# Optimization experiments

Hardware: AMD Instinct MI355X
Metric: run time of the kernel (lower is better)

## Reference

```python
import jax, jax.numpy as jnp
import numpy as np

B, L, T = 4, 512, 4096
HID, NH = 1024, 16
HD = HID // NH
MAX_POS = 4096
BASE = 10000.0


def _cos_sin(dim, max_pos, base):
    inv_freq = 1.0 / base ** (jnp.arange(0, dim, 2, dtype=jnp.float32) / dim)
    t = jnp.arange(max_pos, dtype=jnp.float32)
    freqs = jnp.einsum('i,j->ij', t, inv_freq)
    emb = jnp.concatenate([freqs, freqs], axis=-1)  # [max_pos, dim]
    return jnp.cos(emb), jnp.sin(emb)


def _rotate_half(x):
    x1, x2 = x[..., : x.shape[-1] // 2], x[..., x.shape[-1] // 2:]
    return jnp.concatenate([-x2, x1], axis=-1)


def setup_inputs() -> dict:
    key = jax.random.key(0)
    ks = jax.random.split(key, 12)
    s = 0.02
    inp = {
        'latents': jax.random.normal(ks[0], (B, L, HID), jnp.float32),
        'target': jax.random.normal(ks[1], (B, T, HID), jnp.float32),
        'target_mask': jax.random.randint(ks[2], (B, T), 0, 2).astype(bool),
        'target_timestamp': jnp.sort(jax.random.randint(ks[3], (B, T), 0, MAX_POS), axis=-1),
        'Wq': jax.random.normal(ks[4], (HID, HID), jnp.float32) * s,
        'bq': jnp.zeros((HID,), jnp.float32),
        'Wk': jax.random.normal(ks[5], (HID, HID), jnp.float32) * s,
        'bk': jnp.zeros((HID,), jnp.float32),
        'Wv': jax.random.normal(ks[6], (HID, HID), jnp.float32) * s,
        'bv': jnp.zeros((HID,), jnp.float32),
        'Wo': jax.random.normal(ks[7], (HID, HID), jnp.float32) * s,
        'bo': jnp.zeros((HID,), jnp.float32),
    }
    return inp


def reference(latents, target, target_mask, target_timestamp, Wq, bq, Wk, bk, Wv, bv, Wo, bo):
    cos, sin = _cos_sin(HD, MAX_POS, BASE)  # [MAX_POS, HD]
    # latents_timestamp: arange(L) * (max-1)/(L-1), cast to int
    lat_ts = (jnp.arange(L, dtype=jnp.float32) * (MAX_POS - 1) / (L - 1)).astype(jnp.int64)
    lat_ts = jnp.broadcast_to(lat_ts[None, :], (B, L))

    # QKV projections (torch Linear: x @ W.T + b)
    q = (latents @ Wq.T + bq).reshape(B, L, NH, HD).transpose(0, 2, 1, 3)  # [B,H,L,D]
    k = (target @ Wk.T + bk).reshape(B, T, NH, HD).transpose(0, 2, 1, 3)   # [B,H,T,D]
    v = (target @ Wv.T + bv).reshape(B, T, NH, HD).transpose(0, 2, 1, 3)

    # RoPE with gathered timestamps; unsqueeze over head dim
    cq, sq = cos[lat_ts][:, None], sin[lat_ts][:, None]          # [B,1,L,D]
    ck, sk = cos[target_timestamp][:, None], sin[target_timestamp][:, None]  # [B,1,T,D]
    q = q * cq + _rotate_half(q) * sq
    k = k * ck + _rotate_half(k) * sk

    # SDPA with boolean attn mask (True = attend)
    scores = jnp.einsum('bhld,bhtd->bhlt', q, k) / jnp.sqrt(jnp.float32(HD))
    bias = jnp.where(target_mask[:, None, None, :], 0.0, -jnp.inf).astype(scores.dtype)
    attn = jax.nn.softmax(scores + bias, axis=-1)
    out = jnp.einsum('bhlt,bhtd->bhld', attn, v)  # [B,H,L,D]
    out = out.transpose(0, 2, 1, 3).reshape(B, L, HID)
    return out @ Wo.T + bo
```

## Files before the change

kernel.cpp:

```cpp
#include <hip/hip_runtime.h>

#define B_ 4
#define L_ 512
#define T_ 4096
#define NH_ 16
#define HD_ 64

using f32x4 = __attribute__((ext_vector_type(4))) float;
using bf16x8 = __attribute__((ext_vector_type(8))) short;
using u32x4 = __attribute__((ext_vector_type(4))) unsigned int;

__device__ __forceinline__ unsigned short f2bf(float x) {
  unsigned int u = __builtin_bit_cast(unsigned int, x);
  u += 0x7fffu + ((u >> 16) & 1u);
  return (unsigned short)(u >> 16);
}

__device__ __forceinline__ unsigned cvtpk(float lo, float hi) {
  unsigned r;
  asm("v_cvt_pk_bf16_f32 %0, %1, %2" : "=v"(r) : "v"(lo), "v"(hi));
  return r;
}

__device__ __forceinline__ u32x4 cvt8(const float4& a, const float4& b) {
  u32x4 r;
  r[0] = (unsigned)f2bf(a.x) | ((unsigned)f2bf(a.y) << 16);
  r[1] = (unsigned)f2bf(a.z) | ((unsigned)f2bf(a.w) << 16);
  r[2] = (unsigned)f2bf(b.x) | ((unsigned)f2bf(b.y) << 16);
  r[3] = (unsigned)f2bf(b.z) | ((unsigned)f2bf(b.w) << 16);
  return r;
}

__device__ __forceinline__ void gload16(const void* g, void* l) {
  __builtin_amdgcn_global_load_lds(
      (const __attribute__((address_space(1))) unsigned int*)g,
      (__attribute__((address_space(3))) unsigned int*)l, 16, 0, 0);
}

#define BC8(x) __builtin_bit_cast(bf16x8, (x))

struct CvtArgs {
  const float* src[6];
  unsigned short* dst[6];
  int cum[7];
};

__global__ void cvt_bf16(CvtArgs a, int total, float* __restrict__ cost,
                         float* __restrict__ sint) {
  if (blockIdx.x >= 2048) {
    const int idx = (blockIdx.x - 2048) * 256 + threadIdx.x;
    const int pos = idx >> 5, i = idx & 31;
    const float inv = 1.0f / powf(10000.0f, (float)(2 * i) * (1.0f / 64.0f));
    const float f = (float)pos * inv;
    cost[idx] = cosf(f);
    sint[idx] = sinf(f);
    return;
  }
  for (int g = blockIdx.x * 256 + threadIdx.x; g < total; g += 2048 * 256) {
    int r = 0;
#pragma unroll
    for (int q = 0; q < 5; ++q) r += (g >= a.cum[q + 1]);
    const int lc = g - a.cum[r];
    const float4* s = (const float4*)a.src[r] + (size_t)lc * 2;
    float4 x0 = s[0], x1 = s[1];
    *((u32x4*)a.dst[r] + lc) = cvt8(x0, x1);
  }
}

template <int EPI>
__global__ __launch_bounds__(256, 2) void gemm_bf(
    const unsigned short* __restrict__ A, const unsigned short* __restrict__ Wb,
    const float* __restrict__ bias, void* __restrict__ outp,
    const float* __restrict__ cost, const float* __restrict__ sint,
    const int* __restrict__ ts) {
  __shared__ u32x4 lsA[2][512];
  __shared__ u32x4 lsB[2][512];
  const int tid = threadIdx.x;
  const int mt = blockIdx.x >> 3, nt = blockIdx.x & 7;
  const int mBase = mt << 7, nBase = nt << 7;
  const int lane = tid & 63, wid = tid >> 6;
  const int wr = wid >> 1, wc = wid & 1;
  const int lr = lane & 15, lg = lane >> 4;

  f32x4 acc[4][4];
#pragma unroll
  for (int m = 0; m < 4; ++m)
#pragma unroll
    for (int n = 0; n < 4; ++n) acc[m][n] = (f32x4){0.f, 0.f, 0.f, 0.f};

  auto stage = [&](int bi, int kt) {
    const int ko = kt * 32;
#pragma unroll
    for (int j2 = 0; j2 < 2; ++j2) {
      const int j = wid * 2 + j2;
      const int row = (j & 1) * 64 + lane;
      const int kg = j >> 1;
      gload16(A + (size_t)(mBase + row) * 1024 + ko + kg * 8,
              (unsigned short*)lsA[bi] + j * 512);
      gload16(Wb + (size_t)(nBase + row) * 1024 + ko + kg * 8,
              (unsigned short*)lsB[bi] + j * 512);
    }
  };

  stage(0, 0);
  __syncthreads();
  int cur = 0;
  for (int kt = 0; kt < 32; ++kt) {
    if (kt < 31) stage(cur ^ 1, kt + 1);
    const u32x4* As = lsA[cur];
    const u32x4* Bs = lsB[cur];
    bf16x8 af[4], bfr[4];
#pragma unroll
    for (int m = 0; m < 4; ++m) af[m] = BC8(As[lg * 128 + wr * 64 + m * 16 + lr]);
#pragma unroll
    for (int n = 0; n < 4; ++n) bfr[n] = BC8(Bs[lg * 128 + wc * 64 + n * 16 + lr]);
#pragma unroll
    for (int m = 0; m < 4; ++m)
#pragma unroll
      for (int n = 0; n < 4; ++n)
        acc[m][n] = __builtin_amdgcn_mfma_f32_16x16x32_bf16(af[m], bfr[n], acc[m][n], 0, 0, 0);
    __syncthreads();
    cur ^= 1;
  }

  float bv[4];
#pragma unroll
  for (int n = 0; n < 4; ++n) bv[n] = bias[nBase + wc * 64 + n * 16 + lr];

  if (EPI == 3) {
    float* Of = (float*)outp;
#pragma unroll
    for (int m = 0; m < 4; ++m)
#pragma unroll
      for (int r = 0; r < 4; ++r) {
        const int gR = mBase + wr * 64 + m * 16 + lg * 4 + r;
#pragma unroll
        for (int n = 0; n < 4; ++n)
          Of[(size_t)gR * 1024 + nBase + wc * 64 + n * 16 + lr] = acc[m][n][r] + bv[n];
      }
  } else {
    unsigned short* Qo = (unsigned short*)outp;
    const int h = (nBase >> 6) + wc;
#pragma unroll
    for (int m = 0; m < 4; ++m) {
#pragma unroll
      for (int r = 0; r < 4; ++r) {
        const int gR = mBase + wr * 64 + m * 16 + lg * 4 + r;
        const int b2 = gR >> 9, p2 = gR & 511;
        const int pos = (int)(((float)p2 * 4095.0f) / 511.0f);
        const float* cp = cost + pos * 32;
        const float* sp = sint + pos * 32;
        const size_t obase = (((size_t)(b2 * NH_ + h)) * L_ + p2) * HD_;
#pragma unroll
        for (int n = 0; n < 2; ++n) {
          const int d = n * 16 + lr;
          const float x1 = acc[m][n][r] + bv[n];
          const float x2 = acc[m][n + 2][r] + bv[n + 2];
          const float c = cp[d], s = sp[d];
          Qo[obase + d] = f2bf(x1 * c - x2 * s);
          Qo[obase + d + 32] = f2bf(x2 * c + x1 * s);
        }
      }
    }
  }
}

__global__ __launch_bounds__(256, 3) void gemm_kv3(
    const unsigned short* __restrict__ A, const unsigned short* __restrict__ Wkv,
    const float* __restrict__ bkp, const float* __restrict__ bvp,
    unsigned short* __restrict__ Ko, unsigned short* __restrict__ Vo,
    const float* __restrict__ cost, const float* __restrict__ sint,
    const int* __restrict__ ts) {
  __shared__ u32x4 lsA[2][512];
  __shared__ u32x4 lsB[2][512];
  const int tid = threadIdx.x;
  const int orig = blockIdx.x;
  const int wgid = (orig & 7) * 256 + (orig >> 3);
  const int mt = wgid >> 4, nt = wgid & 15;
  const int mBase = mt << 7, nBase = nt << 7;
  const int lane = tid & 63, wid = tid >> 6;
  const int wr = wid >> 1, wc = wid & 1;
  const int lr = lane & 15, lg = lane >> 4;

  f32x4 acc[4][4];
#pragma unroll
  for (int m = 0; m < 4; ++m)
#pragma unroll
    for (int n = 0; n < 4; ++n) acc[m][n] = (f32x4){0.f, 0.f, 0.f, 0.f};

  auto stage = [&](int bi, int kt) {
    const int ko = kt * 32;
#pragma unroll
    for (int j2 = 0; j2 < 2; ++j2) {
      const int j = wid * 2 + j2;
      const int row = (j & 1) * 64 + lane;
      const int kg = j >> 1;
      gload16(A + (size_t)(mBase + row) * 1024 + ko + kg * 8,
              (unsigned short*)lsA[bi] + j * 512);
      gload16(Wkv + (size_t)(nBase + row) * 1024 + ko + kg * 8,
              (unsigned short*)lsB[bi] + j * 512);
    }
  };

  stage(0, 0);
  __syncthreads();
  int cur = 0;
  for (int kt = 0; kt < 32; ++kt) {
    if (kt < 31) stage(cur ^ 1, kt + 1);
    const u32x4* As = lsA[cur];
    const u32x4* Bs = lsB[cur];
    bf16x8 af[4], bfr[4];
#pragma unroll
    for (int m = 0; m < 4; ++m) af[m] = BC8(As[lg * 128 + wr * 64 + m * 16 + lr]);
#pragma unroll
    for (int n = 0; n < 4; ++n) bfr[n] = BC8(Bs[lg * 128 + wc * 64 + n * 16 + lr]);
#pragma unroll
    for (int m = 0; m < 4; ++m)
#pragma unroll
      for (int n = 0; n < 4; ++n)
        acc[m][n] = __builtin_amdgcn_mfma_f32_16x16x32_bf16(af[m], bfr[n], acc[m][n], 0, 0, 0);
    __syncthreads();
    cur ^= 1;
  }

  const bool isV = (nBase >= 1024);
  const int nb = isV ? (nBase - 1024) : nBase;
  const float* bp = isV ? bvp : bkp;
  const int h = (nb >> 6) + wc;
  float bb[4];
#pragma unroll
  for (int n = 0; n < 4; ++n) bb[n] = bp[nb + wc * 64 + n * 16 + lr];

  if (!isV) {
#pragma unroll
    for (int m = 0; m < 4; ++m) {
#pragma unroll
      for (int r = 0; r < 4; ++r) {
        const int gR = mBase + wr * 64 + m * 16 + lg * 4 + r;
        const int b2 = gR >> 12, p2 = gR & 4095;
        const int pos = ts[gR];
        const float* cp = cost + pos * 32;
        const float* sp = sint + pos * 32;
        const size_t obase = (((size_t)(b2 * NH_ + h)) * T_ + p2) * HD_;
#pragma unroll
        for (int n = 0; n < 2; ++n) {
          const int d = n * 16 + lr;
          const float x1 = acc[m][n][r] + bb[n];
          const float x2 = acc[m][n + 2][r] + bb[n + 2];
          const float c = cp[d], s = sp[d];
          Ko[obase + d] = f2bf(x1 * c - x2 * s);
          Ko[obase + d + 32] = f2bf(x2 * c + x1 * s);
        }
      }
    }
  } else {
#pragma unroll
    for (int m = 0; m < 4; ++m) {
      const int r0 = mBase + wr * 64 + m * 16 + lg * 4;
      const int b = r0 >> 12, t = r0 & 4095;
#pragma unroll
      for (int n = 0; n < 4; ++n) {
        const int d = n * 16 + lr;
        ushort4 pk;
        pk.x = f2bf(acc[m][n][0] + bb[n]);
        pk.y = f2bf(acc[m][n][1] + bb[n]);
        pk.z = f2bf(acc[m][n][2] + bb[n]);
        pk.w = f2bf(acc[m][n][3] + bb[n]);
        *(ushort4*)(Vo + (((size_t)(b * NH_ + h)) * HD_ + d) * (size_t)T_ + t) = pk;
      }
    }
  }
}

#define SCL 0.180336880111f
__global__ __launch_bounds__(512, 4) void attn_full(
    const unsigned short* __restrict__ Q, const unsigned short* __restrict__ K,
    const unsigned short* __restrict__ V, const int* __restrict__ mask,
    unsigned short* __restrict__ O) {
  __shared__ u32x4 QP2[1024];
  __shared__ u32x4 Ksh[2][2][512];
  __shared__ u32x4 Vsh[2][2][512];
  const int tid = threadIdx.x, lane = tid & 63, w = tid >> 6;
  const int half = w >> 2, wsub = w & 3;
  const int lr = lane & 15, lg = lane >> 4;
  const int orig = blockIdx.x;
  const int wg = (orig & 7) * 64 + (orig >> 3);
  const int lt = wg & 7, bh = wg >> 3;
  const int b = bh >> 4;
  const int l0 = lt << 6;
  const int tBase = half << 11;

  gload16(Q + ((size_t)bh * L_ + l0 + lane) * HD_ + w * 8, (unsigned short*)QP2 + w * 512);
  __syncthreads();
  bf16x8 qf[2];
#pragma unroll
  for (int ks2 = 0; ks2 < 2; ++ks2)
    qf[ks2] = BC8(QP2[(ks2 * 4 + lg) * 64 + wsub * 16 + lr]);

  f32x4 po[4];
#pragma unroll
  for (int n = 0; n < 4; ++n) po[n] = (f32x4){0.f, 0.f, 0.f, 0.f};
  float mrun = -1e30f, lrun = 0.f;

  char* Pw = (char*)QP2 + w * 2048;
  const int swz = (lr & 7) << 4;
  const int* mrow = mask + (size_t)b * T_ + tBase;

  auto stage = [&](int bi, int it) {
    const int t0 = tBase + (it << 6);
#pragma unroll
    for (int i = 0; i < 2; ++i) {
      const int li = wsub * 2 + i;
      gload16(K + ((size_t)bh * T_ + t0 + lane) * HD_ + li * 8,
              (unsigned short*)Ksh[half][bi] + li * 512);
      gload16(V + ((size_t)bh * HD_ + lane) * T_ + t0 + li * 8,
              (unsigned short*)Vsh[half][bi] + li * 512);
    }
  };

  stage(0, 0);
  __syncthreads();
  int cur = 0;
  for (int it = 0; it < 32; ++it) {
    if (it < 31) stage(cur ^ 1, it + 1);
    const int t0l = it << 6;

    f32x4 s[4];
#pragma unroll
    for (int n = 0; n < 4; ++n) s[n] = (f32x4){0.f, 0.f, 0.f, 0.f};
#pragma unroll
    for (int ks2 = 0; ks2 < 2; ++ks2) {
#pragma unroll
      for (int n = 0; n < 4; ++n) {
        bf16x8 kb = BC8(Ksh[half][cur][(ks2 * 4 + lg) * 64 + n * 16 + lr]);
        s[n] = __builtin_amdgcn_mfma_f32_16x16x32_bf16(kb, qf[ks2], s[n], 0, 0, 0);
      }
    }
#pragma unroll
    for (int n = 0; n < 4; ++n) {
      const int4 mi = *(const int4*)(mrow + t0l + n * 16 + lg * 4);
      s[n][0] = s[n][0] * SCL + (mi.x ? 0.f : -1e30f);
      s[n][1] = s[n][1] * SCL + (mi.y ? 0.f : -1e30f);
      s[n][2] = s[n][2] * SCL + (mi.z ? 0.f : -1e30f);
      s[n][3] = s[n][3] * SCL + (mi.w ? 0.f : -1e30f);
    }
    f32x4 m4;
#pragma unroll
    for (int r = 0; r < 4; ++r)
      m4[r] = fmaxf(fmaxf(s[0][r], s[1][r]), fmaxf(s[2][r], s[3][r]));
    float x = fmaxf(fmaxf(m4[0], m4[1]), fmaxf(m4[2], m4[3]));
    x = fmaxf(x, __shfl_xor(x, 16));
    x = fmaxf(x, __shfl_xor(x, 32));
    const float mnew = fmaxf(mrun, x);
    const float sc = __builtin_exp2f(mrun - mnew);
    mrun = mnew;
    f32x4 ls4 = (f32x4){0.f, 0.f, 0.f, 0.f};
#pragma unroll
    for (int n = 0; n < 4; ++n)
#pragma unroll
      for (int r = 0; r < 4; ++r) {
        const float p = __builtin_exp2f(s[n][r] - mnew);
        s[n][r] = p;
        ls4[r] += p;
      }
    lrun = lrun * sc + ((ls4[0] + ls4[1]) + (ls4[2] + ls4[3]));
#pragma unroll
    for (int n = 0; n < 4; ++n) po[n] *= sc;
#pragma unroll
    for (int n = 0; n < 4; ++n) {
      uint2 pk;
      pk.x = cvtpk(s[n][0], s[n][1]);
      pk.y = cvtpk(s[n][2], s[n][3]);
      *(uint2*)(Pw + ((lr * 128 + n * 32 + lg * 8) ^ swz)) = pk;
    }
    bf16x8 pa[2];
#pragma unroll
    for (int ks2 = 0; ks2 < 2; ++ks2)
      pa[ks2] = BC8(*(const u32x4*)(Pw + ((lr * 128 + ks2 * 64 + lg * 16) ^ swz)));
#pragma unroll
    for (int ks2 = 0; ks2 < 2; ++ks2) {
#pragma unroll
      for (int n = 0; n < 4; ++n) {
        bf16x8 vb = BC8(Vsh[half][cur][(ks2 * 4 + lg) * 64 + n * 16 + lr]);
        po[n] = __builtin_amdgcn_mfma_f32_16x16x32_bf16(vb, pa[ks2], po[n], 0, 0, 0);
      }
    }
    __syncthreads();
    cur ^= 1;
  }

  lrun += __shfl_xor(lrun, 16);
  lrun += __shfl_xor(lrun, 32);
  const int rl = wsub * 16 + lr;

  float* ex = (float*)Ksh;
  float* ml = (float*)Vsh;
  if (half == 1) {
#pragma unroll
    for (int n = 0; n < 4; ++n) {
      const int idx = rl * 16 + ((n * 4 + lg) ^ (rl & 15));
      *((f32x4*)ex + idx) = po[n];
    }
    if (lg == 0) {
      ml[rl * 2] = mrun;
      ml[rl * 2 + 1] = lrun;
    }
  }
  __syncthreads();
  if (half == 0) {
    const float m1 = ml[rl * 2], l1v = ml[rl * 2 + 1];
    const float M = fmaxf(mrun, m1);
    const float w0 = __builtin_exp2f(mrun - M), w1 = __builtin_exp2f(m1 - M);
    const float inv = 1.0f / (lrun * w0 + l1v * w1);
    const int gl = l0 + rl;
    unsigned short* orow = O + ((size_t)b * L_ + gl) * 1024 + (bh & 15) * HD_;
#pragma unroll
    for (int n = 0; n < 4; ++n) {
      const int idx = rl * 16 + ((n * 4 + lg) ^ (rl & 15));
      const f32x4 p1 = *((f32x4*)ex + idx);
      uint2 pk;
      pk.x = cvtpk((po[n][0] * w0 + p1[0] * w1) * inv, (po[n][1] * w0 + p1[1] * w1) * inv);
      pk.y = cvtpk((po[n][2] * w0 + p1[2] * w1) * inv, (po[n][3] * w0 + p1[3] * w1) * inv);
      *(uint2*)(orow + n * 16 + lg * 4) = pk;
    }
  }
}

extern "C" void kernel_launch(void* const* d_in, const int* in_sizes, int n_in,
                              void* d_out, int out_size, void* d_ws, size_t ws_size,
                              hipStream_t stream) {
  const float* latents = (const float*)d_in[0];
  const float* target = (const float*)d_in[1];
  const int* mask = (const int*)d_in[2];
  const int* ts = (const int*)d_in[3];
  const float* Wq = (const float*)d_in[4];
  const float* bq = (const float*)d_in[5];
  const float* Wk = (const float*)d_in[6];
  const float* bk = (const float*)d_in[7];
  const float* Wv = (const float*)d_in[8];
  const float* bv = (const float*)d_in[9];
  const float* Wo = (const float*)d_in[10];
  const float* bo = (const float*)d_in[11];
  float* out = (float*)d_out;

  char* ws = (char*)d_ws;
  float* cost = (float*)ws;
  float* sint = (float*)(ws + (512 << 10));
  unsigned short* Qws = (unsigned short*)(ws + (1ull << 20));
  unsigned short* Kws = (unsigned short*)(ws + (5ull << 20));
  unsigned short* Vws = (unsigned short*)(ws + (37ull << 20));
  unsigned short* Ows = (unsigned short*)(ws + (69ull << 20));
  unsigned short* latb = (unsigned short*)(ws + (73ull << 20));
  unsigned short* tgtb = (unsigned short*)(ws + (77ull << 20));
  unsigned short* Wqb = (unsigned short*)(ws + (109ull << 20));
  unsigned short* Wkvb = (unsigned short*)(ws + (111ull << 20));
  unsigned short* Wob = (unsigned short*)(ws + (115ull << 20));

  CvtArgs ca;
  ca.src[0] = latents; ca.dst[0] = latb;
  ca.src[1] = target;  ca.dst[1] = tgtb;
  ca.src[2] = Wq;      ca.dst[2] = Wqb;
  ca.src[3] = Wk;      ca.dst[3] = Wkvb;
  ca.src[4] = Wv;      ca.dst[4] = Wkvb + (1 << 20);
  ca.src[5] = Wo;      ca.dst[5] = Wob;
  const int nch[6] = {2097152 / 8, 16777216 / 8, 131072, 131072, 131072, 131072};
  ca.cum[0] = 0;
  for (int i = 0; i < 6; ++i) ca.cum[i + 1] = ca.cum[i] + nch[i];
  const int total = ca.cum[6];

  cvt_bf16<<<dim3(2560), dim3(256), 0, stream>>>(ca, total, cost, sint);
  gemm_bf<0><<<dim3(16 * 8), dim3(256), 0, stream>>>(latb, Wqb, bq, Qws, cost, sint, nullptr);
  gemm_kv3<<<dim3(2048), dim3(256), 0, stream>>>(tgtb, Wkvb, bk, bv, Kws, Vws, cost, sint, ts);
  attn_full<<<dim3(512), dim3(512), 0, stream>>>(Qws, Kws, Vws, mask, Ows);
  gemm_bf<3><<<dim3(16 * 8), dim3(256), 0, stream>>>(Ows, Wob, bo, out, nullptr, nullptr, nullptr);
}
```

Measured before the change: 323.4 us.

## Triple-buffer KV GEMM with single barrier and lazy softmax rescale

The K/V projection GEMM moves from a double buffer to a three-stage LDS ring. It prefetches two tiles ahead and replaces the two __syncthreads per iteration with an explicit vmcnt wait plus one barrier, so global loads overlap MFMA work. Separately, the attention online softmax skips the running-max update and the rescaling of the accumulator and sum unless some row's new max exceeds the old one by more than a threshold. This trades fewer rescale multiplies for exponentials that can reach up to 2^4 before normalisation. The larger LDS footprint in the GEMM may reduce occupancy.

```diff
diff --git a/kernel.cpp b/kernel.cpp
--- a/kernel.cpp
+++ b/kernel.cpp
@@ -165,14 +165,14 @@
   }
 }
 
-__global__ __launch_bounds__(256, 3) void gemm_kv3(
+__global__ __launch_bounds__(256, 3) void gemm_kv4(
     const unsigned short* __restrict__ A, const unsigned short* __restrict__ Wkv,
     const float* __restrict__ bkp, const float* __restrict__ bvp,
     unsigned short* __restrict__ Ko, unsigned short* __restrict__ Vo,
     const float* __restrict__ cost, const float* __restrict__ sint,
     const int* __restrict__ ts) {
-  __shared__ u32x4 lsA[2][512];
-  __shared__ u32x4 lsB[2][512];
+  __shared__ u32x4 lsA[3][512];
+  __shared__ u32x4 lsB[3][512];
   const int tid = threadIdx.x;
   const int orig = blockIdx.x;
   const int wgid = (orig & 7) * 256 + (orig >> 3);
@@ -188,7 +188,8 @@
 #pragma unroll
     for (int n = 0; n < 4; ++n) acc[m][n] = (f32x4){0.f, 0.f, 0.f, 0.f};
 
-  auto stage = [&](int bi, int kt) {
+  auto stage = [&](int kt) {
+    const int bi = kt % 3;
     const int ko = kt * 32;
 #pragma unroll
     for (int j2 = 0; j2 < 2; ++j2) {
@@ -202,25 +203,28 @@
     }
   };
 
-  stage(0, 0);
-  __syncthreads();
-  int cur = 0;
+  stage(0);
+  stage(1);
+
   for (int kt = 0; kt < 32; ++kt) {
-    if (kt < 31) stage(cur ^ 1, kt + 1);
-    const u32x4* As = lsA[cur];
-    const u32x4* Bs = lsB[cur];
+    if (kt == 31)
+      asm volatile("s_waitcnt vmcnt(0)" ::: "memory");
+    else
+      asm volatile("s_waitcnt vmcnt(4)" ::: "memory");
+    __builtin_amdgcn_s_barrier();
+    const u32x4* As = lsA[kt % 3];
+    const u32x4* Bs = lsB[kt % 3];
     bf16x8 af[4], bfr[4];
 #pragma unroll
     for (int m = 0; m < 4; ++m) af[m] = BC8(As[lg * 128 + wr * 64 + m * 16 + lr]);
 #pragma unroll
     for (int n = 0; n < 4; ++n) bfr[n] = BC8(Bs[lg * 128 + wc * 64 + n * 16 + lr]);
+    if (kt < 30) stage(kt + 2);
 #pragma unroll
     for (int m = 0; m < 4; ++m)
 #pragma unroll
       for (int n = 0; n < 4; ++n)
         acc[m][n] = __builtin_amdgcn_mfma_f32_16x16x32_bf16(af[m], bfr[n], acc[m][n], 0, 0, 0);
-    __syncthreads();
-    cur ^= 1;
   }
 
   const bool isV = (nBase >= 1024);
@@ -351,21 +355,24 @@
     float x = fmaxf(fmaxf(m4[0], m4[1]), fmaxf(m4[2], m4[3]));
     x = fmaxf(x, __shfl_xor(x, 16));
     x = fmaxf(x, __shfl_xor(x, 32));
-    const float mnew = fmaxf(mrun, x);
-    const float sc = __builtin_exp2f(mrun - mnew);
-    mrun = mnew;
+    if (!__all(x <= mrun + 4.0f)) {
+      const float mnew = fmaxf(mrun, x);
+      const float sc = __builtin_exp2f(mrun - mnew);
+      mrun = mnew;
+      lrun *= sc;
+#pragma unroll
+      for (int n = 0; n < 4; ++n) po[n] *= sc;
+    }
     f32x4 ls4 = (f32x4){0.f, 0.f, 0.f, 0.f};
 #pragma unroll
     for (int n = 0; n < 4; ++n)
 #pragma unroll
       for (int r = 0; r < 4; ++r) {
-        const float p = __builtin_exp2f(s[n][r] - mnew);
+        const float p = __builtin_exp2f(s[n][r] - mrun);
         s[n][r] = p;
         ls4[r] += p;
       }
-    lrun = lrun * sc + ((ls4[0] + ls4[1]) + (ls4[2] + ls4[3]));
-#pragma unroll
-    for (int n = 0; n < 4; ++n) po[n] *= sc;
+    lrun += ((ls4[0] + ls4[1]) + (ls4[2] + ls4[3]));
 #pragma unroll
     for (int n = 0; n < 4; ++n) {
       uint2 pk;
@@ -470,7 +477,7 @@
 
   cvt_bf16<<<dim3(2560), dim3(256), 0, stream>>>(ca, total, cost, sint);
   gemm_bf<0><<<dim3(16 * 8), dim3(256), 0, stream>>>(latb, Wqb, bq, Qws, cost, sint, nullptr);
-  gemm_kv3<<<dim3(2048), dim3(256), 0, stream>>>(tgtb, Wkvb, bk, bv, Kws, Vws, cost, sint, ts);
+  gemm_kv4<<<dim3(2048), dim3(256), 0, stream>>>(tgtb, Wkvb, bk, bv, Kws, Vws, cost, sint, ts);
   attn_full<<<dim3(512), dim3(512), 0, stream>>>(Qws, Kws, Vws, mask, Ows);
   gemm_bf<3><<<dim3(16 * 8), dim3(256), 0, stream>>>(Ows, Wob, bo, out, nullptr, nullptr, nullptr);
 }
```

Measured after the change: 364.7 us. 1.13x slower.
